# Optimization experiments

Measured on AMD Instinct MI355X. Metric: run time of the kernel, lower is better.

## Reference

```python
import jax, jax.numpy as jnp
import numpy as np

N, IN_DIM, HID, K, TOP_M = 131072, 512, 128, 256, 32


def setup_inputs() -> dict:
    key = jax.random.key(0)
    ks = jax.random.split(key, 16)
    s_in = 1.0 / np.sqrt(IN_DIM)
    s_h = 1.0 / np.sqrt(HID)
    return {
        "h0": jax.random.normal(ks[0], (N, IN_DIM), jnp.float32),
        "W1": jax.random.uniform(ks[1], (IN_DIM, HID), jnp.float32, -s_in, s_in),
        "b1": jax.random.uniform(ks[2], (HID,), jnp.float32, -s_in, s_in),
        "W2": jax.random.uniform(ks[3], (HID, HID), jnp.float32, -s_h, s_h),
        "b2": jax.random.uniform(ks[4], (HID,), jnp.float32, -s_h, s_h),
        "Wm": jax.random.uniform(ks[5], (HID, HID), jnp.float32, -s_h, s_h),
        "bm": jax.random.uniform(ks[6], (HID,), jnp.float32, -s_h, s_h),
        "Wt": jax.random.uniform(ks[7], (HID, HID), jnp.float32, -s_h, s_h),
        "bt": jax.random.uniform(ks[8], (HID,), jnp.float32, -s_h, s_h),
        "Wp": jax.random.uniform(ks[9], (HID, HID), jnp.float32, -s_h, s_h),
        "bp": jax.random.uniform(ks[10], (HID,), jnp.float32, -s_h, s_h),
        "cb_m": jax.random.normal(ks[11], (K, HID), jnp.float32),
        "cb_t": jax.random.normal(ks[12], (K, HID), jnp.float32),
        "cb_p": jax.random.normal(ks[13], (K, HID), jnp.float32),
        "ws": jax.random.uniform(ks[14], (HID,), jnp.float32, -s_h, s_h),
        "wb": jax.random.uniform(ks[15], (1,), jnp.float32, -s_h, s_h),
    }


def _l2n(x):
    return x / jnp.clip(jnp.linalg.norm(x, axis=-1, keepdims=True), 1e-12, None)


def _cos_dist(z, cb):
    # cosine-sim VQ codebook 'distance': [N, K] similarity matrix
    return jnp.einsum("nd,kd->nk", _l2n(z), _l2n(cb))


def reference(h0, W1, b1, W2, b2, Wm, bm, Wt, bt, Wp, bp, cb_m, cb_t, cb_p, ws, wb):
    # encoder MLP
    H = jax.nn.relu(jax.nn.relu(h0 @ W1 + b1) @ W2 + b2)  # [N, HID]
    dist_m = _cos_dist(H @ Wm + bm, cb_m)  # [N, K]
    dist_t = _cos_dist(H @ Wt + bt, cb_t)
    dist_p = _cos_dist(H @ Wp + bp, cb_p)
    # default path: argmin over codebook axis
    k_m = jnp.argmin(dist_m, axis=-1)
    k_t = jnp.argmin(dist_t, axis=-1)
    k_p = jnp.argmin(dist_p, axis=-1)
    codes = jnp.stack([k_m, k_t, k_p], axis=-1)  # [N, 3]
    alpha = jax.nn.sigmoid(H @ ws + wb[0])  # [N]
    n = codes.shape[0]
    M = min(TOP_M, n)
    _, key_idx = jax.lax.top_k(alpha, M)
    key_idx = jnp.clip(key_idx, 0, n - 1)
    return codes, key_idx, codes[key_idx]
```

## Files before the change

kernel.cpp:

```cpp
#include <hip/hip_runtime.h>

#define NROWS   131072
#define INDIM   512
#define HIDD    128
#define KCB     256
#define RPB     128

#define OFF_A     0u
#define OFF_CV    98304u
#define OFF_LOG   99072u
#define OFF_HIST  230144u
#define OFF_META  295680u
#define OFF_LISTA 295696u
#define OFF_LISTB 295824u
#define LISTB_CAP 2048u

__device__ __forceinline__ unsigned order_key(float f) {
    unsigned u = __float_as_uint(f);
    return u ^ ((u & 0x80000000u) ? 0xFFFFFFFFu : 0x80000000u);
}

__global__ __launch_bounds__(256) void vq_precompute(
    const float* __restrict__ Wm, const float* __restrict__ bm,
    const float* __restrict__ Wt, const float* __restrict__ bt,
    const float* __restrict__ Wp, const float* __restrict__ bp,
    const float* __restrict__ cbm, const float* __restrict__ cbt, const float* __restrict__ cbp,
    float* __restrict__ A, float* __restrict__ cv, unsigned* __restrict__ hist)
{
    for (unsigned i = blockIdx.x * 256u + threadIdx.x; i < 65536u + 16u; i += 24u * 256u)
        hist[i] = 0u;

    const int c  = blockIdx.x >> 3;
    const int jg = (blockIdx.x & 7) * 16;
    const float* W  = (c == 0) ? Wm  : (c == 1) ? Wt  : Wp;
    const float* bb = (c == 0) ? bm  : (c == 1) ? bt  : bp;
    const float* cb = (c == 0) ? cbm : (c == 1) ? cbt : cbp;
    const int k = threadIdx.x;
    const float4* cbr = (const float4*)(cb + (size_t)k * HIDD);
    float s = 0.f;
    for (int d = 0; d < HIDD / 4; ++d) {
        float4 x = cbr[d];
        s += x.x * x.x + x.y * x.y + x.z * x.z + x.w * x.w;
    }
    const float rn = 1.f / fmaxf(sqrtf(s), 1e-12f);
    for (int j = jg; j < jg + 16; ++j) {
        const float4* wr = (const float4*)(W + (size_t)j * HIDD);
        float acc = 0.f;
        for (int d = 0; d < HIDD / 4; ++d) {
            float4 x = cbr[d]; float4 w = wr[d];
            acc += x.x * w.x + x.y * w.y + x.z * w.z + x.w * w.w;
        }
        A[((size_t)c * HIDD + j) * KCB + k] = acc * rn;
    }
    if (jg == 0) {
        const float4* br = (const float4*)bb;
        float acc = 0.f;
        for (int d = 0; d < HIDD / 4; ++d) {
            float4 x = cbr[d]; float4 w = br[d];
            acc += x.x * w.x + x.y * w.y + x.z * w.z + x.w * w.w;
        }
        cv[(size_t)c * KCB + k] = acc * rn;
    }
}

__global__ __launch_bounds__(256, 2) void vq_main(
    const float* __restrict__ h0, const float* __restrict__ W1, const float* __restrict__ bias1,
    const float* __restrict__ W2, const float* __restrict__ bias2,
    const float* __restrict__ Amat, const float* __restrict__ cv, const float* __restrict__ wsv,
    int* __restrict__ codes, float* __restrict__ logits, unsigned* __restrict__ hist)
{
    __shared__ float T[HIDD * RPB];
    __shared__ float S[4096];

    const int t  = threadIdx.x;
    const int tx = t & 15;
    const int ty = t >> 4;
    const int row0 = blockIdx.x * RPB;

    {
        float acc[8][8] = {};
        const int srow = t >> 1;
        const int sq   = (t & 1) * 8;
        const float* hp = h0 + (size_t)(row0 + srow) * INDIM + sq;
        for (int kc = 0; kc < INDIM; kc += 16) {
            float4 ha = *(const float4*)(hp + kc);
            float4 hb = *(const float4*)(hp + kc + 4);
            const float4* wsrc = (const float4*)(W1 + (size_t)kc * HIDD);
            float4 w0 = wsrc[t];
            float4 w1 = wsrc[t + 256];
            __syncthreads();
            S[(sq + 0) * RPB + srow] = ha.x;
            S[(sq + 1) * RPB + srow] = ha.y;
            S[(sq + 2) * RPB + srow] = ha.z;
            S[(sq + 3) * RPB + srow] = ha.w;
            S[(sq + 4) * RPB + srow] = hb.x;
            S[(sq + 5) * RPB + srow] = hb.y;
            S[(sq + 6) * RPB + srow] = hb.z;
            S[(sq + 7) * RPB + srow] = hb.w;
            float4* wdst = (float4*)(S + 2048);
            wdst[t]       = w0;
            wdst[t + 256] = w1;
            __syncthreads();
            #pragma unroll
            for (int k = 0; k < 16; ++k) {
                float4 a0 = *(const float4*)&S[k * RPB + 8 * ty];
                float4 a1 = *(const float4*)&S[k * RPB + 8 * ty + 4];
                float4 b0 = *(const float4*)&S[2048 + k * HIDD + 4 * tx];
                float4 b1v = *(const float4*)&S[2048 + k * HIDD + 4 * tx + 64];
                float aa[8] = {a0.x, a0.y, a0.z, a0.w, a1.x, a1.y, a1.z, a1.w};
                float bb[8] = {b0.x, b0.y, b0.z, b0.w, b1v.x, b1v.y, b1v.z, b1v.w};
                #pragma unroll
                for (int r = 0; r < 8; ++r)
                    #pragma unroll
                    for (int j = 0; j < 8; ++j)
                        acc[r][j] = fmaf(aa[r], bb[j], acc[r][j]);
            }
        }
        float4 bv0 = *(const float4*)&bias1[4 * tx];
        float4 bv1 = *(const float4*)&bias1[4 * tx + 64];
        float ba[8] = {bv0.x, bv0.y, bv0.z, bv0.w, bv1.x, bv1.y, bv1.z, bv1.w};
        #pragma unroll
        for (int i = 0; i < 2; ++i)
            #pragma unroll
            for (int j = 0; j < 4; ++j) {
                const int c = 4 * tx + 64 * i + j;
                float4 lo, hi;
                lo.x = fmaxf(acc[0][i * 4 + j] + ba[i * 4 + j], 0.f);
                lo.y = fmaxf(acc[1][i * 4 + j] + ba[i * 4 + j], 0.f);
                lo.z = fmaxf(acc[2][i * 4 + j] + ba[i * 4 + j], 0.f);
                lo.w = fmaxf(acc[3][i * 4 + j] + ba[i * 4 + j], 0.f);
                hi.x = fmaxf(acc[4][i * 4 + j] + ba[i * 4 + j], 0.f);
                hi.y = fmaxf(acc[5][i * 4 + j] + ba[i * 4 + j], 0.f);
                hi.z = fmaxf(acc[6][i * 4 + j] + ba[i * 4 + j], 0.f);
                hi.w = fmaxf(acc[7][i * 4 + j] + ba[i * 4 + j], 0.f);
                *(float4*)&T[c * RPB + 8 * ty]     = lo;
                *(float4*)&T[c * RPB + 8 * ty + 4] = hi;
            }
    }

    {
        float acc[8][8] = {};
        for (int kc = 0; kc < HIDD; kc += 16) {
            const float4* wsrc = (const float4*)(W2 + (size_t)kc * HIDD);
            float4 w0 = wsrc[t];
            float4 w1 = wsrc[t + 256];
            __syncthreads();
            float4* wdst = (float4*)S;
            wdst[t]       = w0;
            wdst[t + 256] = w1;
            __syncthreads();
            #pragma unroll
            for (int k = 0; k < 16; ++k) {
                float4 a0 = *(const float4*)&T[(kc + k) * RPB + 8 * ty];
                float4 a1 = *(const float4*)&T[(kc + k) * RPB + 8 * ty + 4];
                float4 b0 = *(const float4*)&S[k * HIDD + 4 * tx];
                float4 b1v = *(const float4*)&S[k * HIDD + 4 * tx + 64];
                float aa[8] = {a0.x, a0.y, a0.z, a0.w, a1.x, a1.y, a1.z, a1.w};
                float bb[8] = {b0.x, b0.y, b0.z, b0.w, b1v.x, b1v.y, b1v.z, b1v.w};
                #pragma unroll
                for (int r = 0; r < 8; ++r)
                    #pragma unroll
                    for (int j = 0; j < 8; ++j)
                        acc[r][j] = fmaf(aa[r], bb[j], acc[r][j]);
            }
        }
        __syncthreads();
        float4 bv0 = *(const float4*)&bias2[4 * tx];
        float4 bv1 = *(const float4*)&bias2[4 * tx + 64];
        float ba[8] = {bv0.x, bv0.y, bv0.z, bv0.w, bv1.x, bv1.y, bv1.z, bv1.w};
        #pragma unroll
        for (int i = 0; i < 2; ++i)
            #pragma unroll
            for (int j = 0; j < 4; ++j) {
                const int c = 4 * tx + 64 * i + j;
                float4 lo, hi;
                lo.x = fmaxf(acc[0][i * 4 + j] + ba[i * 4 + j], 0.f);
                lo.y = fmaxf(acc[1][i * 4 + j] + ba[i * 4 + j], 0.f);
                lo.z = fmaxf(acc[2][i * 4 + j] + ba[i * 4 + j], 0.f);
                lo.w = fmaxf(acc[3][i * 4 + j] + ba[i * 4 + j], 0.f);
                hi.x = fmaxf(acc[4][i * 4 + j] + ba[i * 4 + j], 0.f);
                hi.y = fmaxf(acc[5][i * 4 + j] + ba[i * 4 + j], 0.f);
                hi.z = fmaxf(acc[6][i * 4 + j] + ba[i * 4 + j], 0.f);
                hi.w = fmaxf(acc[7][i * 4 + j] + ba[i * 4 + j], 0.f);
                *(float4*)&T[c * RPB + 8 * ty]     = lo;
                *(float4*)&T[c * RPB + 8 * ty + 4] = hi;
            }
    }

    for (int cbk = 0; cbk < 3; ++cbk) {
        float acc[8][16] = {};
        for (int kc = 0; kc < HIDD; kc += 16) {
            const float4* src = (const float4*)(Amat + ((size_t)cbk * HIDD + kc) * KCB);
            float4 s0 = src[t];
            float4 s1 = src[t + 256];
            float4 s2 = src[t + 512];
            float4 s3 = src[t + 768];
            __syncthreads();
            float4* dst = (float4*)S;
            dst[t]       = s0;
            dst[t + 256] = s1;
            dst[t + 512] = s2;
            dst[t + 768] = s3;
            __syncthreads();
            #pragma unroll
            for (int k = 0; k < 16; ++k) {
                float4 a0 = *(const float4*)&T[(kc + k) * RPB + 8 * ty];
                float4 a1 = *(const float4*)&T[(kc + k) * RPB + 8 * ty + 4];
                float aa[8] = {a0.x, a0.y, a0.z, a0.w, a1.x, a1.y, a1.z, a1.w};
                #pragma unroll
                for (int i = 0; i < 4; ++i) {
                    float4 bv = *(const float4*)&S[k * KCB + 4 * tx + 64 * i];
                    float bb[4] = {bv.x, bv.y, bv.z, bv.w};
                    #pragma unroll
                    for (int r = 0; r < 8; ++r)
                        #pragma unroll
                        for (int j = 0; j < 4; ++j)
                            acc[r][i * 4 + j] = fmaf(aa[r], bb[j], acc[r][i * 4 + j]);
                }
            }
        }
        float mv[8] = {3.4e38f, 3.4e38f, 3.4e38f, 3.4e38f, 3.4e38f, 3.4e38f, 3.4e38f, 3.4e38f};
        int   mi[8] = {0, 0, 0, 0, 0, 0, 0, 0};
        #pragma unroll
        for (int i = 0; i < 4; ++i) {
            float4 cvv = *(const float4*)&cv[cbk * KCB + 4 * tx + 64 * i];
            float ca[4] = {cvv.x, cvv.y, cvv.z, cvv.w};
            #pragma unroll
            for (int j = 0; j < 4; ++j) {
                const int c = 64 * i + 4 * tx + j;
                #pragma unroll
                for (int r = 0; r < 8; ++r) {
                    float v = acc[r][i * 4 + j] + ca[j];
                    if (v < mv[r]) { mv[r] = v; mi[r] = c; }
                }
            }
        }
        #pragma unroll
        for (int d = 1; d < 16; d <<= 1) {
            #pragma unroll
            for (int r = 0; r < 8; ++r) {
                float ov = __shfl_xor(mv[r], d);
                int   oi = __shfl_xor(mi[r], d);
                if (ov < mv[r] || (ov == mv[r] && oi < mi[r])) { mv[r] = ov; mi[r] = oi; }
            }
        }
        if (tx == 0) {
            #pragma unroll
            for (int r = 0; r < 8; ++r)
                codes[(size_t)(row0 + 8 * ty + r) * 3 + cbk] = mi[r];
        }
    }

    __syncthreads();
    if (t < HIDD) S[t] = wsv[t];
    __syncthreads();
    if (t < RPB) {
        float s = 0.f;
        #pragma unroll 8
        for (int k = 0; k < HIDD; ++k) s = fmaf(T[k * RPB + t], S[k], s);
        logits[row0 + t] = s;
        atomicAdd(&hist[order_key(s) >> 16], 1u);
    }
}

__global__ __launch_bounds__(1024) void vq_findp(const unsigned* __restrict__ hist,
                                                 unsigned* __restrict__ meta)
{
    __shared__ unsigned Tb[1024];
    __shared__ unsigned sIg, sPg;
    const int t = threadIdx.x;
    unsigned s = 0;
    const uint4* hv = (const uint4*)(hist + (size_t)t * 64);
    for (int j = 0; j < 16; ++j) { uint4 h = hv[j]; s += h.x + h.y + h.z + h.w; }
    Tb[t] = s;
    __syncthreads();
    for (int d = 1; d < 1024; d <<= 1) {
        unsigned v = (t + d < 1024) ? Tb[t + d] : 0u;
        __syncthreads();
        Tb[t] += v;
        __syncthreads();
    }
    const unsigned Ti = Tb[t];
    const unsigned P  = Ti - s;
    if (P < 32u && Ti >= 32u) { sIg = (unsigned)t; sPg = P; }
    __syncthreads();
    const int ig = (int)sIg;
    const unsigned Pg = sPg;
    if (t < 64) {
        unsigned c = hist[ig * 64 + t];
        unsigned Tw = c;
        #pragma unroll
        for (int d = 1; d < 64; d <<= 1) {
            unsigned v = __shfl_down(Tw, d);
            if (t + d < 64) Tw += v;
        }
        unsigned Pl = Pg + Tw - c;
        if (Pl < 32u && Pl + c >= 32u) { meta[2] = (unsigned)(ig * 64 + t); meta[3] = Pl; }
    }
}

__global__ __launch_bounds__(256) void vq_collect(
    const float* __restrict__ logits, unsigned* __restrict__ meta,
    unsigned* __restrict__ listA, unsigned* __restrict__ listB)
{
    const int i = blockIdx.x * 256 + threadIdx.x;
    const unsigned key = order_key(logits[i]);
    const unsigned p = meta[2];
    const unsigned b = key >> 16;
    if (b > p) {
        unsigned idx = atomicAdd(&meta[0], 1u);
        if (idx < 64u) { listA[2 * idx] = key; listA[2 * idx + 1] = (unsigned)i; }
    } else if (b == p) {
        unsigned idx = atomicAdd(&meta[1], 1u);
        if (idx < LISTB_CAP) { listB[2 * idx] = key; listB[2 * idx + 1] = (unsigned)i; }
    }
}

__global__ __launch_bounds__(256) void vq_final(
    const unsigned* __restrict__ meta,
    const unsigned* __restrict__ listA, const unsigned* __restrict__ listB,
    const int* __restrict__ codes,
    int* __restrict__ outki, int* __restrict__ outsel)
{
    __shared__ unsigned Ks[64 + LISTB_CAP];
    __shared__ unsigned Is[64 + LISTB_CAP];
    __shared__ int sel[32];
    const int t = threadIdx.x;
    const unsigned nAv = meta[0];
    const unsigned nBv = meta[1];
    const int nA = (nAv > 64u) ? 64 : (int)nAv;
    const int nB = (nBv > LISTB_CAP) ? (int)LISTB_CAP : (int)nBv;
    const int n  = nA + nB;
    for (int j = t; j < n; j += 256) {
        if (j < nA) { Ks[j] = listA[2 * j]; Is[j] = listA[2 * j + 1]; }
        else        { int jj = j - nA; Ks[j] = listB[2 * jj]; Is[j] = listB[2 * jj + 1]; }
    }
    __syncthreads();
    for (int j = t; j < n; j += 256) {
        const unsigned kj = Ks[j], ij = Is[j];
        int rank = 0;
        for (int m = 0; m < n; ++m) {
            const unsigned km = Ks[m], im = Is[m];
            rank += (km > kj) || (km == kj && im < ij);
        }
        if (rank < 32) sel[rank] = (int)ij;
    }
    __syncthreads();
    if (t < 32) outki[t] = sel[t];
    if (t < 96) outsel[t] = codes[3 * sel[t / 3] + (t % 3)];
}

extern "C" void kernel_launch(void* const* d_in, const int* in_sizes, int n_in,
                              void* d_out, int out_size, void* d_ws, size_t ws_size,
                              hipStream_t stream)
{
    (void)in_sizes; (void)n_in; (void)out_size; (void)ws_size;

    const float* h0  = (const float*)d_in[0];
    const float* W1  = (const float*)d_in[1];
    const float* b1  = (const float*)d_in[2];
    const float* W2  = (const float*)d_in[3];
    const float* b2  = (const float*)d_in[4];
    const float* Wm  = (const float*)d_in[5];
    const float* bm  = (const float*)d_in[6];
    const float* Wt  = (const float*)d_in[7];
    const float* bt  = (const float*)d_in[8];
    const float* Wp  = (const float*)d_in[9];
    const float* bp  = (const float*)d_in[10];
    const float* cbm = (const float*)d_in[11];
    const float* cbt = (const float*)d_in[12];
    const float* cbp = (const float*)d_in[13];
    const float* wsv = (const float*)d_in[14];

    float*    wsf   = (float*)d_ws;
    unsigned* wsu   = (unsigned*)d_ws;
    float*    A     = wsf + OFF_A;
    float*    cvv   = wsf + OFF_CV;
    float*    logit = wsf + OFF_LOG;
    unsigned* hist  = wsu + OFF_HIST;
    unsigned* meta  = wsu + OFF_META;
    unsigned* listA = wsu + OFF_LISTA;
    unsigned* listB = wsu + OFF_LISTB;

    int* codes  = (int*)d_out;
    int* outki  = codes + (size_t)NROWS * 3;
    int* outsel = outki + 32;

    vq_precompute<<<24, 256, 0, stream>>>(Wm, bm, Wt, bt, Wp, bp, cbm, cbt, cbp, A, cvv, hist);
    vq_main<<<NROWS / RPB, 256, 0, stream>>>(h0, W1, b1, W2, b2, A, cvv, wsv, codes, logit, hist);
    vq_findp<<<1, 1024, 0, stream>>>(hist, meta);
    vq_collect<<<NROWS / 256, 256, 0, stream>>>(logit, meta, listA, listB);
    vq_final<<<1, 256, 0, stream>>>(meta, listA, listB, codes, outki, outsel);
}
```

Measured before the change: 714.6 us.

## Read weights directly from global/L1 instead of staging through LDS in vq_main

The W1, W2 and codebook-projection operands are now read directly from global memory, relying on L1/L2 caching, instead of being cooperatively copied into shared memory each chunk. The h0 tile is double-buffered in LDS with a register prefetch, which removes one barrier per chunk. The codebook matmul is split into two 128-column halves so the per-thread accumulator shrinks from 8x16 to 8x8, and the launch_bounds min-blocks hint is dropped. This is meant to cut LDS traffic and synchronisation, but it puts more load on the vector-memory path and caches and may change register allocation and occupancy.

```diff
diff --git a/kernel.cpp b/kernel.cpp
--- a/kernel.cpp
+++ b/kernel.cpp
@@ -63,7 +63,7 @@
     }
 }
 
-__global__ __launch_bounds__(256, 2) void vq_main(
+__global__ __launch_bounds__(256) void vq_main(
     const float* __restrict__ h0, const float* __restrict__ W1, const float* __restrict__ bias1,
     const float* __restrict__ W2, const float* __restrict__ bias2,
     const float* __restrict__ Amat, const float* __restrict__ cv, const float* __restrict__ wsv,
@@ -82,33 +82,32 @@
         const int srow = t >> 1;
         const int sq   = (t & 1) * 8;
         const float* hp = h0 + (size_t)(row0 + srow) * INDIM + sq;
+        float4 ha = *(const float4*)(hp);
+        float4 hb = *(const float4*)(hp + 4);
         for (int kc = 0; kc < INDIM; kc += 16) {
-            float4 ha = *(const float4*)(hp + kc);
-            float4 hb = *(const float4*)(hp + kc + 4);
-            const float4* wsrc = (const float4*)(W1 + (size_t)kc * HIDD);
-            float4 w0 = wsrc[t];
-            float4 w1 = wsrc[t + 256];
+            float* Sb = S + ((kc >> 4) & 1) * 2048;
+            Sb[(sq + 0) * RPB + srow] = ha.x;
+            Sb[(sq + 1) * RPB + srow] = ha.y;
+            Sb[(sq + 2) * RPB + srow] = ha.z;
+            Sb[(sq + 3) * RPB + srow] = ha.w;
+            Sb[(sq + 4) * RPB + srow] = hb.x;
+            Sb[(sq + 5) * RPB + srow] = hb.y;
+            Sb[(sq + 6) * RPB + srow] = hb.z;
+            Sb[(sq + 7) * RPB + srow] = hb.w;
             __syncthreads();
-            S[(sq + 0) * RPB + srow] = ha.x;
-            S[(sq + 1) * RPB + srow] = ha.y;
-            S[(sq + 2) * RPB + srow] = ha.z;
-            S[(sq + 3) * RPB + srow] = ha.w;
-            S[(sq + 4) * RPB + srow] = hb.x;
-            S[(sq + 5) * RPB + srow] = hb.y;
-            S[(sq + 6) * RPB + srow] = hb.z;
-            S[(sq + 7) * RPB + srow] = hb.w;
-            float4* wdst = (float4*)(S + 2048);
-            wdst[t]       = w0;
-            wdst[t + 256] = w1;
-            __syncthreads();
-            #pragma unroll
+            if (kc + 16 < INDIM) {
+                ha = *(const float4*)(hp + kc + 16);
+                hb = *(const float4*)(hp + kc + 20);
+            }
+            const float* Wb = W1 + (size_t)kc * HIDD + 4 * tx;
+            #pragma unroll 4
             for (int k = 0; k < 16; ++k) {
-                float4 a0 = *(const float4*)&S[k * RPB + 8 * ty];
-                float4 a1 = *(const float4*)&S[k * RPB + 8 * ty + 4];
-                float4 b0 = *(const float4*)&S[2048 + k * HIDD + 4 * tx];
-                float4 b1v = *(const float4*)&S[2048 + k * HIDD + 4 * tx + 64];
+                float4 a0 = *(const float4*)&Sb[k * RPB + 8 * ty];
+                float4 a1 = *(const float4*)&Sb[k * RPB + 8 * ty + 4];
+                float4 b0 = *(const float4*)(Wb + k * HIDD);
+                float4 b1 = *(const float4*)(Wb + k * HIDD + 64);
                 float aa[8] = {a0.x, a0.y, a0.z, a0.w, a1.x, a1.y, a1.z, a1.w};
-                float bb[8] = {b0.x, b0.y, b0.z, b0.w, b1v.x, b1v.y, b1v.z, b1v.w};
+                float bb[8] = {b0.x, b0.y, b0.z, b0.w, b1.x, b1.y, b1.z, b1.w};
                 #pragma unroll
                 for (int r = 0; r < 8; ++r)
                     #pragma unroll
@@ -137,32 +136,24 @@
                 *(float4*)&T[c * RPB + 8 * ty + 4] = hi;
             }
     }
+    __syncthreads();
 
     {
         float acc[8][8] = {};
-        for (int kc = 0; kc < HIDD; kc += 16) {
-            const float4* wsrc = (const float4*)(W2 + (size_t)kc * HIDD);
-            float4 w0 = wsrc[t];
-            float4 w1 = wsrc[t + 256];
-            __syncthreads();
-            float4* wdst = (float4*)S;
-            wdst[t]       = w0;
-            wdst[t + 256] = w1;
-            __syncthreads();
-            #pragma unroll
-            for (int k = 0; k < 16; ++k) {
-                float4 a0 = *(const float4*)&T[(kc + k) * RPB + 8 * ty];
-                float4 a1 = *(const float4*)&T[(kc + k) * RPB + 8 * ty + 4];
-                float4 b0 = *(const float4*)&S[k * HIDD + 4 * tx];
-                float4 b1v = *(const float4*)&S[k * HIDD + 4 * tx + 64];
-                float aa[8] = {a0.x, a0.y, a0.z, a0.w, a1.x, a1.y, a1.z, a1.w};
-                float bb[8] = {b0.x, b0.y, b0.z, b0.w, b1v.x, b1v.y, b1v.z, b1v.w};
+        const float* Wb = W2 + 4 * tx;
+        #pragma unroll 4
+        for (int k = 0; k < HIDD; ++k) {
+            float4 a0 = *(const float4*)&T[k * RPB + 8 * ty];
+            float4 a1 = *(const float4*)&T[k * RPB + 8 * ty + 4];
+            float4 b0 = *(const float4*)(Wb + k * HIDD);
+            float4 b1 = *(const float4*)(Wb + k * HIDD + 64);
+            float aa[8] = {a0.x, a0.y, a0.z, a0.w, a1.x, a1.y, a1.z, a1.w};
+            float bb[8] = {b0.x, b0.y, b0.z, b0.w, b1.x, b1.y, b1.z, b1.w};
+            #pragma unroll
+            for (int r = 0; r < 8; ++r)
                 #pragma unroll
-                for (int r = 0; r < 8; ++r)
-                    #pragma unroll
-                    for (int j = 0; j < 8; ++j)
-                        acc[r][j] = fmaf(aa[r], bb[j], acc[r][j]);
-            }
+                for (int j = 0; j < 8; ++j)
+                    acc[r][j] = fmaf(aa[r], bb[j], acc[r][j]);
         }
         __syncthreads();
         float4 bv0 = *(const float4*)&bias2[4 * tx];
@@ -186,54 +177,45 @@
                 *(float4*)&T[c * RPB + 8 * ty + 4] = hi;
             }
     }
+    __syncthreads();
+    if (t < HIDD) S[t] = wsv[t];
 
     for (int cbk = 0; cbk < 3; ++cbk) {
-        float acc[8][16] = {};
-        for (int kc = 0; kc < HIDD; kc += 16) {
-            const float4* src = (const float4*)(Amat + ((size_t)cbk * HIDD + kc) * KCB);
-            float4 s0 = src[t];
-            float4 s1 = src[t + 256];
-            float4 s2 = src[t + 512];
-            float4 s3 = src[t + 768];
-            __syncthreads();
-            float4* dst = (float4*)S;
-            dst[t]       = s0;
-            dst[t + 256] = s1;
-            dst[t + 512] = s2;
-            dst[t + 768] = s3;
-            __syncthreads();
-            #pragma unroll
-            for (int k = 0; k < 16; ++k) {
-                float4 a0 = *(const float4*)&T[(kc + k) * RPB + 8 * ty];
-                float4 a1 = *(const float4*)&T[(kc + k) * RPB + 8 * ty + 4];
-                float aa[8] = {a0.x, a0.y, a0.z, a0.w, a1.x, a1.y, a1.z, a1.w};
-                #pragma unroll
-                for (int i = 0; i < 4; ++i) {
-                    float4 bv = *(const float4*)&S[k * KCB + 4 * tx + 64 * i];
-                    float bb[4] = {bv.x, bv.y, bv.z, bv.w};
-                    #pragma unroll
-                    for (int r = 0; r < 8; ++r)
-                        #pragma unroll
-                        for (int j = 0; j < 4; ++j)
-                            acc[r][i * 4 + j] = fmaf(aa[r], bb[j], acc[r][i * 4 + j]);
-                }
-            }
-        }
         float mv[8] = {3.4e38f, 3.4e38f, 3.4e38f, 3.4e38f, 3.4e38f, 3.4e38f, 3.4e38f, 3.4e38f};
         int   mi[8] = {0, 0, 0, 0, 0, 0, 0, 0};
-        #pragma unroll
-        for (int i = 0; i < 4; ++i) {
-            float4 cvv = *(const float4*)&cv[cbk * KCB + 4 * tx + 64 * i];
-            float ca[4] = {cvv.x, cvv.y, cvv.z, cvv.w};
-            #pragma unroll
-            for (int j = 0; j < 4; ++j) {
-                const int c = 64 * i + 4 * tx + j;
+        #pragma unroll 1
+        for (int half = 0; half < 2; ++half) {
+            float acc[8][8] = {};
+            const float* Ab = Amat + (size_t)cbk * HIDD * KCB + 128 * half + 4 * tx;
+            #pragma unroll 4
+            for (int k = 0; k < HIDD; ++k) {
+                float4 a0 = *(const float4*)&T[k * RPB + 8 * ty];
+                float4 a1 = *(const float4*)&T[k * RPB + 8 * ty + 4];
+                float4 b0 = *(const float4*)(Ab + (size_t)k * KCB);
+                float4 b1 = *(const float4*)(Ab + (size_t)k * KCB + 64);
+                float aa[8] = {a0.x, a0.y, a0.z, a0.w, a1.x, a1.y, a1.z, a1.w};
+                float bb[8] = {b0.x, b0.y, b0.z, b0.w, b1.x, b1.y, b1.z, b1.w};
                 #pragma unroll
-                for (int r = 0; r < 8; ++r) {
-                    float v = acc[r][i * 4 + j] + ca[j];
-                    if (v < mv[r]) { mv[r] = v; mi[r] = c; }
+                for (int r = 0; r < 8; ++r)
+                    #pragma unroll
+                    for (int j = 0; j < 8; ++j)
+                        acc[r][j] = fmaf(aa[r], bb[j], acc[r][j]);
+            }
+            const float* cvb = cv + cbk * KCB + 128 * half + 4 * tx;
+            float4 c0 = *(const float4*)cvb;
+            float4 c1 = *(const float4*)(cvb + 64);
+            float ca[8] = {c0.x, c0.y, c0.z, c0.w, c1.x, c1.y, c1.z, c1.w};
+            #pragma unroll
+            for (int i = 0; i < 2; ++i)
+                #pragma unroll
+                for (int j = 0; j < 4; ++j) {
+                    const int c = 128 * half + 64 * i + 4 * tx + j;
+                    #pragma unroll
+                    for (int r = 0; r < 8; ++r) {
+                        float v = acc[r][4 * i + j] + ca[4 * i + j];
+                        if (v < mv[r]) { mv[r] = v; mi[r] = c; }
+                    }
                 }
-            }
         }
         #pragma unroll
         for (int d = 1; d < 16; d <<= 1) {
@@ -251,8 +233,6 @@
         }
     }
 
-    __syncthreads();
-    if (t < HIDD) S[t] = wsv[t];
     __syncthreads();
     if (t < RPB) {
         float s = 0.f;
```

New measurement: 739.5 us. +3.5%, slower.

## Split codebook GEMM into two column halves to cut accumulator registers

Applied to the files above, without the earlier changes.

The codebook-similarity GEMM is restructured to process the 256 codes in two halves of 128, so each thread holds an 8x8 accumulator instead of 8x16. The running argmin is carried across halves. The min-2-waves launch bound is dropped, and a barrier is added after the T tile is written. Fewer live registers are meant to avoid spills or allow better scheduling. In exchange the T tile is read twice from shared memory and there are twice as many staging barriers.

```diff
diff --git a/kernel.cpp b/kernel.cpp
--- a/kernel.cpp
+++ b/kernel.cpp
@@ -5,6 +5,7 @@
 #define HIDD    128
 #define KCB     256
 #define RPB     128
+#define THREADS 256
 
 #define OFF_A     0u
 #define OFF_CV    98304u
@@ -63,7 +64,7 @@
     }
 }
 
-__global__ __launch_bounds__(256, 2) void vq_main(
+__global__ __launch_bounds__(THREADS) void vq_main(
     const float* __restrict__ h0, const float* __restrict__ W1, const float* __restrict__ bias1,
     const float* __restrict__ W2, const float* __restrict__ bias2,
     const float* __restrict__ Amat, const float* __restrict__ cv, const float* __restrict__ wsv,
@@ -186,54 +187,52 @@
                 *(float4*)&T[c * RPB + 8 * ty + 4] = hi;
             }
     }
+    __syncthreads();
 
     for (int cbk = 0; cbk < 3; ++cbk) {
-        float acc[8][16] = {};
-        for (int kc = 0; kc < HIDD; kc += 16) {
-            const float4* src = (const float4*)(Amat + ((size_t)cbk * HIDD + kc) * KCB);
-            float4 s0 = src[t];
-            float4 s1 = src[t + 256];
-            float4 s2 = src[t + 512];
-            float4 s3 = src[t + 768];
-            __syncthreads();
-            float4* dst = (float4*)S;
-            dst[t]       = s0;
-            dst[t + 256] = s1;
-            dst[t + 512] = s2;
-            dst[t + 768] = s3;
-            __syncthreads();
-            #pragma unroll
-            for (int k = 0; k < 16; ++k) {
-                float4 a0 = *(const float4*)&T[(kc + k) * RPB + 8 * ty];
-                float4 a1 = *(const float4*)&T[(kc + k) * RPB + 8 * ty + 4];
-                float aa[8] = {a0.x, a0.y, a0.z, a0.w, a1.x, a1.y, a1.z, a1.w};
+        float mv[8] = {3.4e38f, 3.4e38f, 3.4e38f, 3.4e38f, 3.4e38f, 3.4e38f, 3.4e38f, 3.4e38f};
+        int   mi[8] = {0, 0, 0, 0, 0, 0, 0, 0};
+        #pragma unroll 1
+        for (int half = 0; half < 2; ++half) {
+            const float* Ab = Amat + (size_t)cbk * HIDD * KCB + 128 * half;
+            float acc[8][8] = {};
+            for (int kc = 0; kc < HIDD; kc += 16) {
+                float4 s0 = *(const float4*)(Ab + (size_t)(kc + (t >> 5)) * KCB + ((t & 31) << 2));
+                float4 s1 = *(const float4*)(Ab + (size_t)(kc + (t >> 5) + 8) * KCB + ((t & 31) << 2));
+                __syncthreads();
+                *(float4*)&S[(t >> 5) * 128 + ((t & 31) << 2)]       = s0;
+                *(float4*)&S[((t >> 5) + 8) * 128 + ((t & 31) << 2)] = s1;
+                __syncthreads();
                 #pragma unroll
-                for (int i = 0; i < 4; ++i) {
-                    float4 bv = *(const float4*)&S[k * KCB + 4 * tx + 64 * i];
-                    float bb[4] = {bv.x, bv.y, bv.z, bv.w};
+                for (int k = 0; k < 16; ++k) {
+                    float4 a0 = *(const float4*)&T[(kc + k) * RPB + 8 * ty];
+                    float4 a1 = *(const float4*)&T[(kc + k) * RPB + 8 * ty + 4];
+                    float4 b0 = *(const float4*)&S[k * 128 + 4 * tx];
+                    float4 b1v = *(const float4*)&S[k * 128 + 4 * tx + 64];
+                    float aa[8] = {a0.x, a0.y, a0.z, a0.w, a1.x, a1.y, a1.z, a1.w};
+                    float bb[8] = {b0.x, b0.y, b0.z, b0.w, b1v.x, b1v.y, b1v.z, b1v.w};
                     #pragma unroll
                     for (int r = 0; r < 8; ++r)
                         #pragma unroll
-                        for (int j = 0; j < 4; ++j)
-                            acc[r][i * 4 + j] = fmaf(aa[r], bb[j], acc[r][i * 4 + j]);
+                        for (int j = 0; j < 8; ++j)
+                            acc[r][j] = fmaf(aa[r], bb[j], acc[r][j]);
                 }
             }
-        }
-        float mv[8] = {3.4e38f, 3.4e38f, 3.4e38f, 3.4e38f, 3.4e38f, 3.4e38f, 3.4e38f, 3.4e38f};
-        int   mi[8] = {0, 0, 0, 0, 0, 0, 0, 0};
-        #pragma unroll
-        for (int i = 0; i < 4; ++i) {
-            float4 cvv = *(const float4*)&cv[cbk * KCB + 4 * tx + 64 * i];
-            float ca[4] = {cvv.x, cvv.y, cvv.z, cvv.w};
-            #pragma unroll
-            for (int j = 0; j < 4; ++j) {
-                const int c = 64 * i + 4 * tx + j;
+            const float* cvb = cv + cbk * KCB + 128 * half;
+            float4 c0 = *(const float4*)(cvb + 4 * tx);
+            float4 c1 = *(const float4*)(cvb + 4 * tx + 64);
+            float ca[8] = {c0.x, c0.y, c0.z, c0.w, c1.x, c1.y, c1.z, c1.w};
+            #pragma unroll
+            for (int i = 0; i < 2; ++i)
                 #pragma unroll
-                for (int r = 0; r < 8; ++r) {
-                    float v = acc[r][i * 4 + j] + ca[j];
-                    if (v < mv[r]) { mv[r] = v; mi[r] = c; }
+                for (int j = 0; j < 4; ++j) {
+                    const int c = 128 * half + 64 * i + 4 * tx + j;
+                    #pragma unroll
+                    for (int r = 0; r < 8; ++r) {
+                        float v = acc[r][i * 4 + j] + ca[i * 4 + j];
+                        if (v < mv[r]) { mv[r] = v; mi[r] = c; }
+                    }
                 }
-            }
         }
         #pragma unroll
         for (int d = 1; d < 16; d <<= 1) {
@@ -387,7 +386,7 @@
     int* outsel = outki + 32;
 
     vq_precompute<<<24, 256, 0, stream>>>(Wm, bm, Wt, bt, Wp, bp, cbm, cbt, cbp, A, cvv, hist);
-    vq_main<<<NROWS / RPB, 256, 0, stream>>>(h0, W1, b1, W2, b2, A, cvv, wsv, codes, logit, hist);
+    vq_main<<<NROWS / RPB, THREADS, 0, stream>>>(h0, W1, b1, W2, b2, A, cvv, wsv, codes, logit, hist);
     vq_findp<<<1, 1024, 0, stream>>>(hist, meta);
     vq_collect<<<NROWS / 256, 256, 0, stream>>>(logit, meta, listA, listB);
     vq_final<<<1, 256, 0, stream>>>(meta, listA, listB, codes, outki, outsel);
```

Result: slower. 822.4 us (+15.1%).
